# Optimization experiments

Measured on AMD Instinct MI355X. Metric: run time of the kernel, lower is better.

## Reference

```python
import jax, jax.numpy as jnp
import numpy as np

B, S, D, F, E = 1, 1024, 1024, 4096, 8  # batch, seq, embed_dim, ffn_dim, num_experts(workers)
EPS = 1e-5


def setup_inputs() -> dict:
    key = jax.random.key(0)
    ks = jax.random.split(key, 4)
    x = jax.random.normal(ks[0], (B, S, D), jnp.float32)
    # expert centroids (orthogonal init gain 0.1 in original; scaled normal is fine for a reference)
    centroids = jax.random.normal(ks[1], (E, D), jnp.float32) * 0.1
    # per-expert BaseSublayer params (LayerNorm + ff1 + ff2); torch Linear convention W:[out,in]
    gamma = jnp.ones((E, D), jnp.float32)
    beta = jnp.zeros((E, D), jnp.float32)
    W1 = jax.random.normal(ks[2], (E, F, D), jnp.float32) * 0.02
    b1 = jnp.zeros((E, F), jnp.float32)
    W2 = jax.random.normal(ks[3], (E, D, F), jnp.float32) * 0.02  # zero-init in original; random for testing
    b2 = jnp.zeros((E, D), jnp.float32)
    return {"x": x, "centroids": centroids, "gamma": gamma, "beta": beta,
            "W1": W1, "b1": b1, "W2": W2, "b2": b2}


def _sublayer(xs, g, b, W1e, b1e, W2e, b2e):
    # BaseSublayer: xs + ff2(relu(ff1(LN(xs))))
    mu = jnp.mean(xs, axis=-1, keepdims=True)
    var = jnp.mean(jnp.square(xs - mu), axis=-1, keepdims=True)
    h = (xs - mu) * jax.lax.rsqrt(var + EPS) * g + b
    return xs + jax.nn.relu(h @ W1e.T + b1e) @ W2e.T + b2e


def reference(x, centroids, gamma, beta, W1, b1, W2, b2):
    feats = x.reshape(-1, x.shape[-1])                      # [T, D]
    # affinity matmul is under torch.no_grad in the original -> stop_gradient
    scores = jax.lax.stop_gradient(feats @ centroids.T)     # [T, E]
    expert = jnp.argmax(scores, axis=1)                     # greedy top-1 assignment
    onehot = jax.nn.one_hot(expert, E, dtype=feats.dtype)   # [T, E]
    # sigmoid gate: alpha = sigmoid(x . centroid[expert(x)])
    alpha = jax.nn.sigmoid(jnp.sum(feats * centroids[expert], axis=-1, keepdims=True))
    # run each expert's sublayer over all tokens, combine by assignment (dense reference
    # for the sort/gather dispatch + scatter combine of the original)
    ys = jax.vmap(_sublayer, in_axes=(None, 0, 0, 0, 0, 0, 0))(
        feats, gamma, beta, W1, b1, W2, b2)                 # [E, T, D]
    y = jnp.einsum('te,etd->td', onehot, ys)                # [T, D]
    out = alpha * y + (1.0 - alpha) * feats
    return out.reshape(x.shape)
```

## Files before the change

### kernel.cpp

```cpp
#include <hip/hip_runtime.h>
#include <hip/hip_bf16.h>

#define TOK 1024
#define DIM 1024
#define FF  4096
#define NE  8
#define EPSV 1e-5f
#define BUCKET_STRIDE 1040
#define MAXT 16
#define NKC 4
#define KC  (FF / NKC)
#define BK  128

typedef __attribute__((ext_vector_type(8))) short short8;
typedef __attribute__((ext_vector_type(4))) short bfx4;
typedef __attribute__((ext_vector_type(4))) float floatx4;

#define OFF_HNORM  0
#define OFF_H1     (OFF_HNORM + (size_t)TOK*DIM*2)
#define OFF_PART   (OFF_H1 + (size_t)TOK*FF*2)
#define OFF_ALPHA  (OFF_PART + (size_t)NKC*TOK*DIM*4)
#define OFF_EID    (OFF_ALPHA + TOK*4)
#define OFF_CNT    (OFF_EID + TOK*4)
#define OFF_NT     (OFF_CNT + NE*4)
#define OFF_TILES  (OFF_NT + 4)
#define OFF_BUCKET (OFF_TILES + 64*4)
#define OFF_FLAGS  (OFF_BUCKET + NE*BUCKET_STRIDE*4)

struct Ptr8 { const void* p[8]; };

__device__ __forceinline__ float ldf(const void* p, size_t i, int f32) {
    if (f32) return ((const float*)p)[i];
    union { unsigned u; float f; } v;
    v.u = ((unsigned)((const unsigned short*)p)[i]) << 16;
    return v.f;
}

__device__ __forceinline__ short bf16rne(float f) {
    unsigned u = __float_as_uint(f);
    return (short)((u + 0x7FFFu + ((u >> 16) & 1u)) >> 16);
}

__device__ __forceinline__ void stout(void* p, size_t i, float v, int f32) {
    if (f32) ((float*)p)[i] = v;
    else ((__hip_bfloat16*)p)[i] = __float2bfloat16(v);
}

__global__ void k_init(Ptr8 ptrs, int* __restrict__ cnt, int* __restrict__ flags) {
    const int tid = threadIdx.x;
    if (tid < NE) cnt[tid] = 0;
    if (tid < 8) {
        const unsigned* w = (const unsigned*)ptrs.p[tid];
        int f32 = 0;
        for (int i = 0; i < 64; i++) {
            const unsigned v = w[i];
            if (v == 0x3F800000u) { f32 = 1; break; }
            const unsigned lo = v & 0xFFFFu;
            if (lo != 0) {
                const unsigned e = (lo >> 7) & 0xFFu;
                if (e < 0x60u || e > 0x9Fu) { f32 = 1; break; }
            }
        }
        flags[tid] = f32;
    }
    __syncthreads();
    if (tid == 0) {
        int o = 0;
        for (int i = 0; i < 8; i++) o |= flags[i];
        flags[8] = o;
    }
}

__global__ __launch_bounds__(256) void k_route_ln(
    const void* __restrict__ x,
    const void* __restrict__ cent,
    const void* __restrict__ gamma,
    const void* __restrict__ beta,
    const int* __restrict__ flags,
    __hip_bfloat16* __restrict__ hnorm,
    float* __restrict__ alpha,
    int* __restrict__ eid,
    int* __restrict__ cnt,
    int* __restrict__ bucket)
{
    __shared__ float centS[NE * DIM];
    __shared__ float part[4][10];
    __shared__ float bc[3];

    const int tid = threadIdx.x;
    const int t = blockIdx.x;
    const int fx = flags[0], fc = flags[1], fg = flags[2], fb = flags[3];

    for (int i = tid; i < NE * DIM; i += 256) centS[i] = ldf(cent, i, fc);

    float xv[4];
    #pragma unroll
    for (int i = 0; i < 4; i++)
        xv[i] = ldf(x, (size_t)t * DIM + tid + 256 * i, fx);

    __syncthreads();

    float s = 0.f, sq = 0.f, c[NE];
    #pragma unroll
    for (int e = 0; e < NE; e++) c[e] = 0.f;

    #pragma unroll
    for (int i = 0; i < 4; i++) {
        const int d = tid + 256 * i;
        const float f = xv[i];
        s += f; sq += f * f;
        #pragma unroll
        for (int e = 0; e < NE; e++)
            c[e] += f * centS[e * DIM + d];
    }

    #pragma unroll
    for (int o = 32; o > 0; o >>= 1) {
        s  += __shfl_xor(s, o);
        sq += __shfl_xor(sq, o);
        #pragma unroll
        for (int e = 0; e < NE; e++) c[e] += __shfl_xor(c[e], o);
    }
    const int wid = tid >> 6, lid = tid & 63;
    if (lid == 0) {
        part[wid][0] = s; part[wid][1] = sq;
        #pragma unroll
        for (int e = 0; e < NE; e++) part[wid][2 + e] = c[e];
    }
    __syncthreads();

    if (tid == 0) {
        float S = 0.f, SQ = 0.f, C[NE];
        #pragma unroll
        for (int e = 0; e < NE; e++) C[e] = 0.f;
        for (int w = 0; w < 4; w++) {
            S += part[w][0]; SQ += part[w][1];
            #pragma unroll
            for (int e = 0; e < NE; e++) C[e] += part[w][2 + e];
        }
        const float mu = S / (float)DIM;
        const float var = SQ / (float)DIM - mu * mu;
        const float rstd = rsqrtf(var + EPSV);
        int be = 0; float bs = C[0];
        #pragma unroll
        for (int e = 1; e < NE; e++)
            if (C[e] > bs) { bs = C[e]; be = e; }
        alpha[t] = 1.f / (1.f + expf(-bs));
        eid[t] = be;
        const int pos = atomicAdd(&cnt[be], 1);
        bucket[be * BUCKET_STRIDE + pos] = t;
        bc[0] = mu; bc[1] = rstd; bc[2] = __int_as_float(be);
    }
    __syncthreads();

    const float mu = bc[0], rstd = bc[1];
    const int e = __float_as_int(bc[2]);
    #pragma unroll
    for (int i = 0; i < 4; i++) {
        const int d = tid + 256 * i;
        const float g = ldf(gamma, (size_t)e * DIM + d, fg);
        const float b = ldf(beta,  (size_t)e * DIM + d, fb);
        const float h = (xv[i] - mu) * rstd * g + b;
        hnorm[(size_t)t * DIM + d] = __float2bfloat16(h);
    }
}

__global__ void k_plan(const int* __restrict__ cnt, int* __restrict__ bucket,
                       int* __restrict__ tiles, int* __restrict__ numTiles)
{
    if (threadIdx.x == 0 && blockIdx.x == 0) {
        int nt = 0;
        for (int e = 0; e < NE; e++) {
            const int n = cnt[e];
            const int mt = (n + 127) >> 7;
            const int fill = (n > 0) ? bucket[e * BUCKET_STRIDE] : 0;
            for (int i = n; i < mt * 128; i++) bucket[e * BUCKET_STRIDE + i] = fill;
            for (int i = 0; i < mt; i++) tiles[nt++] = (e << 16) | (i * 128);
        }
        *numTiles = nt;
    }
}


template<int FW>
__device__ __forceinline__ void stage_load(const char* W, long rowbase, long rowlen,
                                           int kb, int t, floatx4* wf, short8* wb)
{
    if (FW) {
        #pragma unroll
        for (int r = 0; r < 8; r++) {
            const int row = r * 8 + (t >> 5);
            wf[r] = *(const floatx4*)(W + ((rowbase + row) * rowlen + kb) * 4
                                        + (size_t)(t & 31) * 16);
        }
    } else {
        #pragma unroll
        for (int r = 0; r < 4; r++) {
            const int row = r * 16 + (t >> 4);
            wb[r] = *(const short8*)(W + ((rowbase + row) * rowlen + kb) * 2
                                       + (size_t)(t & 15) * 16);
        }
    }
}

template<int FW>
__device__ __forceinline__ void stage_write(char* buf, int t,
                                            const floatx4* wf, const short8* wb)
{
    if (FW) {
        const int s = (t & 31) >> 1;
        const int h = (t & 1) * 8;
        #pragma unroll
        for (int r = 0; r < 8; r++) {
            const int row = r * 8 + (t >> 5);
            bfx4 v;
            #pragma unroll
            for (int j = 0; j < 4; j++) v[j] = bf16rne(wf[r][j]);
            *(bfx4*)(buf + row * 256 + ((s ^ (row & 15)) << 4) + h) = v;
        }
    } else {
        const int s = t & 15;
        #pragma unroll
        for (int r = 0; r < 4; r++) {
            const int row = r * 16 + (t >> 4);
            *(short8*)(buf + row * 256 + ((s ^ (row & 15)) << 4)) = wb[r];
        }
    }
}

__device__ __forceinline__ short8 ldB(const char* lb, int row, int ks, int q) {
    const int s = ks * 4 + q;
    return *(const short8*)(lb + row * 256 + ((s ^ (row & 15)) << 4));
}

template<int FW>
__device__ __forceinline__ void ff1_core(
    const short* __restrict__ hnorm,
    const void* __restrict__ W1,
    const void* __restrict__ b1, const int fB,
    __hip_bfloat16* __restrict__ h1,
    const int* __restrict__ tiles, const int nt,
    const int* __restrict__ cnt, const int* __restrict__ bucket,
    char (*ldsB)[16384])
{
    const int bid = blockIdx.x;
    const int tile = bid >> 6;
    if (tile >= nt) return;
    const int nb = bid & 63;
    const int td = tiles[tile];
    const int e = td >> 16;
    const int mbase = td & 0xffff;
    const int ne = cnt[e];

    const int tid = threadIdx.x;
    const int wid = tid >> 6, lane = tid & 63;
    const int mr = lane & 15, q = lane >> 4;

    const int m0 = mbase + wid * 32;
    const int n0 = nb * 64;

    const short* Ap[2];
    #pragma unroll
    for (int am = 0; am < 2; am++) {
        const int tok = bucket[e * BUCKET_STRIDE + m0 + am * 16 + mr];
        Ap[am] = hnorm + (size_t)tok * DIM + q * 8;
    }

    floatx4 acc[2][4];
    #pragma unroll
    for (int am = 0; am < 2; am++)
        #pragma unroll
        for (int an = 0; an < 4; an++) acc[am][an] = (floatx4){0.f, 0.f, 0.f, 0.f};

    const long rowbase = (long)e * FF + n0;

    floatx4 wf[8]; short8 wb[4];
    stage_load<FW>((const char*)W1, rowbase, DIM, 0, tid, wf, wb);
    stage_write<FW>(ldsB[0], tid, wf, wb);
    __syncthreads();

    int cur = 0;
    for (int kt = 0; kt < DIM / BK; kt++) {
        short8 Areg[4][2];
        #pragma unroll
        for (int ks = 0; ks < 4; ks++)
            #pragma unroll
            for (int am = 0; am < 2; am++)
                Areg[ks][am] = *(const short8*)(Ap[am] + kt * BK + ks * 32);

        if (kt + 1 < DIM / BK)
            stage_load<FW>((const char*)W1, rowbase, DIM, (kt + 1) * BK, tid, wf, wb);

        const char* lb = ldsB[cur];
        #pragma unroll
        for (int ks = 0; ks < 4; ks++) {
            short8 b[4];
            #pragma unroll
            for (int an = 0; an < 4; an++) b[an] = ldB(lb, an * 16 + mr, ks, q);
            #pragma unroll
            for (int am = 0; am < 2; am++)
                #pragma unroll
                for (int an = 0; an < 4; an++)
                    acc[am][an] = __builtin_amdgcn_mfma_f32_16x16x32_bf16(Areg[ks][am], b[an], acc[am][an], 0, 0, 0);
        }

        if (kt + 1 < DIM / BK)
            stage_write<FW>(ldsB[cur ^ 1], tid, wf, wb);
        __syncthreads();
        cur ^= 1;
    }

    #pragma unroll
    for (int am = 0; am < 2; am++) {
        #pragma unroll
        for (int r = 0; r < 4; r++) {
            const int slot = m0 + am * 16 + q * 4 + r;
            if (slot < ne) {
                const int tr = bucket[e * BUCKET_STRIDE + slot];
                #pragma unroll
                for (int an = 0; an < 4; an++) {
                    const int f = n0 + an * 16 + mr;
                    float v = acc[am][an][r] + ldf(b1, (size_t)e * FF + f, fB);
                    v = v > 0.f ? v : 0.f;
                    h1[(size_t)tr * FF + f] = __float2bfloat16(v);
                }
            }
        }
    }
}

__global__ __launch_bounds__(256, 3) void k_ff1(
    const __hip_bfloat16* __restrict__ hnorm,
    const void* __restrict__ W1,
    const void* __restrict__ b1,
    const int* __restrict__ flags,
    __hip_bfloat16* __restrict__ h1,
    const int* __restrict__ tiles,
    const int* __restrict__ numTiles,
    const int* __restrict__ cnt,
    const int* __restrict__ bucket)
{
    __shared__ char ldsB[2][16384];
    const int nt = *numTiles;
    if (flags[4]) ff1_core<1>((const short*)hnorm, W1, b1, flags[5], h1, tiles, nt, cnt, bucket, ldsB);
    else          ff1_core<0>((const short*)hnorm, W1, b1, flags[5], h1, tiles, nt, cnt, bucket, ldsB);
}

template<int FW>
__device__ __forceinline__ void ff2_core(
    const short* __restrict__ h1,
    const void* __restrict__ W2,
    float* __restrict__ part,
    const int* __restrict__ tiles, const int nt,
    const int* __restrict__ cnt, const int* __restrict__ bucket,
    char (*ldsB)[16384])
{
    const int bid = blockIdx.x;
    const int tile = bid >> 6;
    if (tile >= nt) return;
    const int nb = (bid >> 2) & 15;
    const int kc = bid & 3;
    const int td = tiles[tile];
    const int e = td >> 16;
    const int mbase = td & 0xffff;
    const int ne = cnt[e];

    const int tid = threadIdx.x;
    const int wid = tid >> 6, lane = tid & 63;
    const int mr = lane & 15, q = lane >> 4;

    const int m0 = mbase + wid * 32;
    const int n0 = nb * 64;
    const int kbase = kc * KC;

    const short* Ap[2];
    #pragma unroll
    for (int am = 0; am < 2; am++) {
        const int tok = bucket[e * BUCKET_STRIDE + m0 + am * 16 + mr];
        Ap[am] = h1 + (size_t)tok * FF + kbase + q * 8;
    }

    floatx4 acc[2][4];
    #pragma unroll
    for (int am = 0; am < 2; am++)
        #pragma unroll
        for (int an = 0; an < 4; an++) acc[am][an] = (floatx4){0.f, 0.f, 0.f, 0.f};

    const long rowbase = (long)e * DIM + n0;

    floatx4 wf[8]; short8 wb[4];
    stage_load<FW>((const char*)W2, rowbase, FF, kbase, tid, wf, wb);
    stage_write<FW>(ldsB[0], tid, wf, wb);
    __syncthreads();

    int cur = 0;
    for (int kt = 0; kt < KC / BK; kt++) {
        short8 Areg[4][2];
        #pragma unroll
        for (int ks = 0; ks < 4; ks++)
            #pragma unroll
            for (int am = 0; am < 2; am++)
                Areg[ks][am] = *(const short8*)(Ap[am] + kt * BK + ks * 32);

        if (kt + 1 < KC / BK)
            stage_load<FW>((const char*)W2, rowbase, FF, kbase + (kt + 1) * BK, tid, wf, wb);

        const char* lb = ldsB[cur];
        #pragma unroll
        for (int ks = 0; ks < 4; ks++) {
            short8 b[4];
            #pragma unroll
            for (int an = 0; an < 4; an++) b[an] = ldB(lb, an * 16 + mr, ks, q);
            #pragma unroll
            for (int am = 0; am < 2; am++)
                #pragma unroll
                for (int an = 0; an < 4; an++)
                    acc[am][an] = __builtin_amdgcn_mfma_f32_16x16x32_bf16(Areg[ks][am], b[an], acc[am][an], 0, 0, 0);
        }

        if (kt + 1 < KC / BK)
            stage_write<FW>(ldsB[cur ^ 1], tid, wf, wb);
        __syncthreads();
        cur ^= 1;
    }

    float* pk = part + (size_t)kc * TOK * DIM;
    #pragma unroll
    for (int am = 0; am < 2; am++) {
        #pragma unroll
        for (int r = 0; r < 4; r++) {
            const int slot = m0 + am * 16 + q * 4 + r;
            if (slot < ne) {
                const int tr = bucket[e * BUCKET_STRIDE + slot];
                #pragma unroll
                for (int an = 0; an < 4; an++) {
                    const int d = n0 + an * 16 + mr;
                    pk[(size_t)tr * DIM + d] = acc[am][an][r];
                }
            }
        }
    }
}

__global__ __launch_bounds__(256, 3) void k_ff2(
    const __hip_bfloat16* __restrict__ h1,
    const void* __restrict__ W2,
    const int* __restrict__ flags,
    float* __restrict__ part,
    const int* __restrict__ tiles,
    const int* __restrict__ numTiles,
    const int* __restrict__ cnt,
    const int* __restrict__ bucket)
{
    __shared__ char ldsB[2][16384];
    const int nt = *numTiles;
    if (flags[6]) ff2_core<1>((const short*)h1, W2, part, tiles, nt, cnt, bucket, ldsB);
    else          ff2_core<0>((const short*)h1, W2, part, tiles, nt, cnt, bucket, ldsB);
}

__global__ __launch_bounds__(256) void k_out(
    const float* __restrict__ part,
    const void* __restrict__ b2,
    const void* __restrict__ x,
    const int* __restrict__ flags,
    const float* __restrict__ alpha,
    const int* __restrict__ eid,
    void* __restrict__ out)
{
    const int t = blockIdx.x;
    const int tid = threadIdx.x;
    const int fB = flags[7], fx = flags[0], fo = flags[8];
    const int e = eid[t];
    const float al = alpha[t];
    const int d0 = tid * 4;

    floatx4 s = (floatx4){0.f, 0.f, 0.f, 0.f};
    #pragma unroll
    for (int kc = 0; kc < NKC; kc++) {
        const floatx4 p = *(const floatx4*)(part + (size_t)kc * TOK * DIM + (size_t)t * DIM + d0);
        s[0] += p[0]; s[1] += p[1]; s[2] += p[2]; s[3] += p[3];
    }
    #pragma unroll
    for (int j = 0; j < 4; j++) {
        const int d = d0 + j;
        const float xb = ldf(x, (size_t)t * DIM + d, fx);
        const float v = xb + al * (s[j] + ldf(b2, (size_t)e * DIM + d, fB));
        stout(out, (size_t)t * DIM + d, v, fo);
    }
}

extern "C" void kernel_launch(void* const* d_in, const int* in_sizes, int n_in,
                              void* d_out, int out_size, void* d_ws, size_t ws_size,
                              hipStream_t stream) {
    char* ws = (char*)d_ws;
    Ptr8 ptrs;
    for (int i = 0; i < 8; i++) ptrs.p[i] = d_in[i];

    __hip_bfloat16* hnorm = (__hip_bfloat16*)(ws + OFF_HNORM);
    __hip_bfloat16* h1    = (__hip_bfloat16*)(ws + OFF_H1);
    float* part           = (float*)(ws + OFF_PART);
    float* alpha          = (float*)(ws + OFF_ALPHA);
    int* eid              = (int*)(ws + OFF_EID);
    int* cnt              = (int*)(ws + OFF_CNT);
    int* numTiles         = (int*)(ws + OFF_NT);
    int* tiles            = (int*)(ws + OFF_TILES);
    int* bucket           = (int*)(ws + OFF_BUCKET);
    int* flags            = (int*)(ws + OFF_FLAGS);

    k_init<<<1, 64, 0, stream>>>(ptrs, cnt, flags);
    k_route_ln<<<TOK, 256, 0, stream>>>(d_in[0], d_in[1], d_in[2], d_in[3], flags,
                                        hnorm, alpha, eid, cnt, bucket);
    k_plan<<<1, 64, 0, stream>>>(cnt, bucket, tiles, numTiles);
    k_ff1<<<MAXT * 64, 256, 0, stream>>>(hnorm, d_in[4], d_in[5], flags, h1,
                                         tiles, numTiles, cnt, bucket);
    k_ff2<<<MAXT * 64, 256, 0, stream>>>(h1, d_in[6], flags, part,
                                         tiles, numTiles, cnt, bucket);
    k_out<<<TOK, 256, 0, stream>>>(part, d_in[7], d_in[0], flags, alpha, eid, d_out);
}
```

Before: 384.3 us.

## Route one token per wavefront, reorder MoE GEMM block mapping, raise occupancy

```diff
diff --git a/kernel.cpp b/kernel.cpp
--- a/kernel.cpp
+++ b/kernel.cpp
@@ -84,19 +84,18 @@
     int* __restrict__ bucket)
 {
     __shared__ float centS[NE * DIM];
-    __shared__ float part[4][10];
-    __shared__ float bc[3];
 
     const int tid = threadIdx.x;
-    const int t = blockIdx.x;
+    const int wid = tid >> 6, lid = tid & 63;
+    const int t = blockIdx.x * 4 + wid;
     const int fx = flags[0], fc = flags[1], fg = flags[2], fb = flags[3];
 
     for (int i = tid; i < NE * DIM; i += 256) centS[i] = ldf(cent, i, fc);
 
-    float xv[4];
-    #pragma unroll
-    for (int i = 0; i < 4; i++)
-        xv[i] = ldf(x, (size_t)t * DIM + tid + 256 * i, fx);
+    float xv[16];
+    #pragma unroll
+    for (int i = 0; i < 16; i++)
+        xv[i] = ldf(x, (size_t)t * DIM + lid + 64 * i, fx);
 
     __syncthreads();
 
@@ -105,8 +104,8 @@
     for (int e = 0; e < NE; e++) c[e] = 0.f;
 
     #pragma unroll
-    for (int i = 0; i < 4; i++) {
-        const int d = tid + 256 * i;
+    for (int i = 0; i < 16; i++) {
+        const int d = lid + 64 * i;
         const float f = xv[i];
         s += f; sq += f * f;
         #pragma unroll
@@ -121,45 +120,30 @@
         #pragma unroll
         for (int e = 0; e < NE; e++) c[e] += __shfl_xor(c[e], o);
     }
-    const int wid = tid >> 6, lid = tid & 63;
+
+    int be = 0; float bs = c[0];
+    #pragma unroll
+    for (int e = 1; e < NE; e++)
+        if (c[e] > bs) { bs = c[e]; be = e; }
+    be = __shfl(be, 0); bs = __shfl(bs, 0);
+    s  = __shfl(s, 0);  sq = __shfl(sq, 0);
+
+    const float mu = s / (float)DIM;
+    const float var = sq / (float)DIM - mu * mu;
+    const float rstd = rsqrtf(var + EPSV);
+
     if (lid == 0) {
-        part[wid][0] = s; part[wid][1] = sq;
-        #pragma unroll
-        for (int e = 0; e < NE; e++) part[wid][2 + e] = c[e];
-    }
-    __syncthreads();
-
-    if (tid == 0) {
-        float S = 0.f, SQ = 0.f, C[NE];
-        #pragma unroll
-        for (int e = 0; e < NE; e++) C[e] = 0.f;
-        for (int w = 0; w < 4; w++) {
-            S += part[w][0]; SQ += part[w][1];
-            #pragma unroll
-            for (int e = 0; e < NE; e++) C[e] += part[w][2 + e];
-        }
-        const float mu = S / (float)DIM;
-        const float var = SQ / (float)DIM - mu * mu;
-        const float rstd = rsqrtf(var + EPSV);
-        int be = 0; float bs = C[0];
-        #pragma unroll
-        for (int e = 1; e < NE; e++)
-            if (C[e] > bs) { bs = C[e]; be = e; }
         alpha[t] = 1.f / (1.f + expf(-bs));
         eid[t] = be;
         const int pos = atomicAdd(&cnt[be], 1);
         bucket[be * BUCKET_STRIDE + pos] = t;
-        bc[0] = mu; bc[1] = rstd; bc[2] = __int_as_float(be);
-    }
-    __syncthreads();
-
-    const float mu = bc[0], rstd = bc[1];
-    const int e = __float_as_int(bc[2]);
-    #pragma unroll
-    for (int i = 0; i < 4; i++) {
-        const int d = tid + 256 * i;
-        const float g = ldf(gamma, (size_t)e * DIM + d, fg);
-        const float b = ldf(beta,  (size_t)e * DIM + d, fb);
+    }
+
+    #pragma unroll
+    for (int i = 0; i < 16; i++) {
+        const int d = lid + 64 * i;
+        const float g = ldf(gamma, (size_t)be * DIM + d, fg);
+        const float b = ldf(beta,  (size_t)be * DIM + d, fb);
         const float h = (xv[i] - mu) * rstd * g + b;
         hnorm[(size_t)t * DIM + d] = __float2bfloat16(h);
     }
@@ -244,9 +228,9 @@
     char (*ldsB)[16384])
 {
     const int bid = blockIdx.x;
-    const int tile = bid >> 6;
+    const int tile = bid & 15;
     if (tile >= nt) return;
-    const int nb = bid & 63;
+    const int nb = bid >> 4;
     const int td = tiles[tile];
     const int e = td >> 16;
     const int mbase = td & 0xffff;
@@ -329,7 +313,7 @@
     }
 }
 
-__global__ __launch_bounds__(256, 3) void k_ff1(
+__global__ __launch_bounds__(256, 4) void k_ff1(
     const __hip_bfloat16* __restrict__ hnorm,
     const void* __restrict__ W1,
     const void* __restrict__ b1,
@@ -356,10 +340,10 @@
     char (*ldsB)[16384])
 {
     const int bid = blockIdx.x;
-    const int tile = bid >> 6;
+    const int tile = bid & 15;
     if (tile >= nt) return;
-    const int nb = (bid >> 2) & 15;
-    const int kc = bid & 3;
+    const int kc = (bid >> 4) & 3;
+    const int nb = bid >> 6;
     const int td = tiles[tile];
     const int e = td >> 16;
     const int mbase = td & 0xffff;
@@ -442,7 +426,7 @@
     }
 }
 
-__global__ __launch_bounds__(256, 3) void k_ff2(
+__global__ __launch_bounds__(256, 4) void k_ff2(
     const __hip_bfloat16* __restrict__ h1,
     const void* __restrict__ W2,
     const int* __restrict__ flags,
@@ -508,8 +492,8 @@
     int* flags            = (int*)(ws + OFF_FLAGS);
 
     k_init<<<1, 64, 0, stream>>>(ptrs, cnt, flags);
-    k_route_ln<<<TOK, 256, 0, stream>>>(d_in[0], d_in[1], d_in[2], d_in[3], flags,
-                                        hnorm, alpha, eid, cnt, bucket);
+    k_route_ln<<<TOK / 4, 256, 0, stream>>>(d_in[0], d_in[1], d_in[2], d_in[3], flags,
+                                            hnorm, alpha, eid, cnt, bucket);
     k_plan<<<1, 64, 0, stream>>>(cnt, bucket, tiles, numTiles);
     k_ff1<<<MAXT * 64, 256, 0, stream>>>(hnorm, d_in[4], d_in[5], flags, h1,
                                          tiles, numTiles, cnt, bucket);
```

After: 408.9 us. 6.4% more time.
